# Kernel tuning notes

Measured on AMD Instinct MI355X. Metric: run time of the kernel, lower is better.

## Reference

```python
import jax, jax.numpy as jnp
import numpy as np

L, H, D, N, M, P, C, IMG, B = 12, 12, 768, 197, 3072, 16, 3, 224, 16
SKIP_AT = (3, 6, 9, 12)


def pos_emb(n, d):
    i = jnp.arange(n, dtype=jnp.float32)[:, None]
    j = jnp.arange(d)[None, :]
    je = (j // 2) * 2  # j for even, j-1 for odd
    ang = i / jnp.power(10000.0, je.astype(jnp.float32) / d)
    return jnp.where(j % 2 == 0, jnp.sin(ang), jnp.cos(ang))  # [n, d]


def layer_norm(x, g, b):
    mu = x.mean(-1, keepdims=True)
    var = x.var(-1, keepdims=True)
    return (x - mu) / jnp.sqrt(var + 1e-5) * g + b


def setup_inputs() -> dict:
    key = jax.random.key(0)
    ks = jax.random.split(key, 16)
    s = 0.02
    f32 = jnp.float32
    return {
        "images": jax.random.normal(ks[0], (B, C, IMG, IMG), f32),
        "class_token": jax.random.uniform(ks[1], (1, D), f32),
        "Wp": jax.random.normal(ks[2], (D, P * P * C), f32) * s,
        "bp": jnp.zeros((D,), f32),
        "Wq": jax.random.normal(ks[3], (L, H, D, D), f32) * s,
        "bq": jnp.zeros((L, H, D), f32),
        "Wk": jax.random.normal(ks[4], (L, H, D, D), f32) * s,
        "bk": jnp.zeros((L, H, D), f32),
        "Wv": jax.random.normal(ks[5], (L, H, D, D), f32) * s,
        "bv": jnp.zeros((L, H, D), f32),
        "Wm": jax.random.normal(ks[6], (L, N, H * N), f32) * s,
        "bm": jnp.zeros((L, N), f32),
        "g1": jnp.ones((L, D), f32),
        "be1": jnp.zeros((L, D), f32),
        "W1": jax.random.normal(ks[7], (L, M, D), f32) * s,
        "b1": jnp.zeros((L, M), f32),
        "W2": jax.random.normal(ks[8], (L, D, M), f32) * s,
        "b2": jnp.zeros((L, D), f32),
        "g2": jnp.ones((L, D), f32),
        "be2": jnp.zeros((L, D), f32),
    }


def reference(images, class_token, Wp, bp, Wq, bq, Wk, bk, Wv, bv, Wm, bm,
              g1, be1, W1, b1, W2, b2, g2, be2):
    b = images.shape[0]
    Hn, Wn = IMG // P, IMG // P
    # einops 'b c (patch_x h) (patch_y w) -> b (h w) (patch_x patch_y c)'
    x = images.reshape(b, C, P, Hn, P, Wn).transpose(0, 3, 5, 2, 4, 1)
    patches = x.reshape(b, Hn * Wn, P * P * C)
    tokens = patches @ Wp.T + bp  # [b, N-1, D]
    cls = jnp.broadcast_to(class_token[None], (b, 1, D))
    out = jnp.concatenate([cls, tokens], axis=1) + pos_emb(N, D)[None]
    scale = 1.0 / jnp.sqrt(jnp.float32(N - 1))
    skips = []
    for l in range(L):
        x0 = out
        q = jnp.einsum('bnd,hed->bhne', x0, Wq[l]) + bq[l][None, :, None, :]
        k = jnp.einsum('bnd,hed->bhne', x0, Wk[l]) + bk[l][None, :, None, :]
        v = jnp.einsum('bnd,hed->bhne', x0, Wv[l]) + bv[l][None, :, None, :]
        attn = jax.nn.softmax(jnp.einsum('bhne,bhme->bhnm', q, k) * scale, axis=-1)
        o = jnp.einsum('bhnm,bhme->bhne', attn, v).reshape(b, H * N, D)
        # transpose -> [b, D, H*N], Linear(H*N -> N), transpose back
        msa = jnp.einsum('bfd,nf->bnd', o, Wm[l]) + bm[l][None, :, None]
        x1 = layer_norm(x0 + msa, g1[l], be1[l])
        hdn = jax.nn.gelu(x1 @ W1[l].T + b1[l], approximate=False)
        out = layer_norm(x1 + (hdn @ W2[l].T + b2[l]), g2[l], be2[l])
        if l + 1 in SKIP_AT:
            skips.append(out[:, 1:, :])
    return (out[:, 1:, :], *skips)
```

## Files before the change

kernel.cpp:

```cpp
#include <hip/hip_runtime.h>
#include <cstdint>
#include <cstddef>

typedef __bf16 bf16;
typedef __bf16 bf16x8 __attribute__((ext_vector_type(8)));
typedef float f32x4 __attribute__((ext_vector_type(4)));

#define DEVINL __device__ __forceinline__

typedef const __attribute__((address_space(1))) void* as1cv;
typedef __attribute__((address_space(3))) void* as3v;

DEVINL void gload16(const bf16* g, bf16* l) {
    __builtin_amdgcn_global_load_lds((as1cv)g, (as3v)l, 16, 0, 0);
}

static constexpr int Lh = 12, Hh = 12, Dh = 768, Nh = 197, Mh = 3072, Bh = 16;
static constexpr int BN   = Bh * Nh;
static constexpr int NPAT = Bh * 196;
static constexpr int HD   = Hh * Dh;
static constexpr int QKN  = 2 * HD;
static constexpr int QKV3 = 3 * HD;
static constexpr int NP   = 256;
static constexpr int FHN  = Hh * Nh;
static constexpr int FP   = 2368;
static constexpr size_t SEC = (size_t)Bh * 196 * Dh;
static constexpr long LS3 = (long)QKV3 * Dh;
static constexpr long PART = (long)BN * Dh;

template<int AF32, int BF32, int OUTBF, int BIAS, int ACT, int ZFILL>
__global__ __launch_bounds__(256, 4) void gemm_bt(
    const void* __restrict__ Av, long sAy, long sAz, int lda,
    const void* __restrict__ Bv, long sBy, long sBz, int ldb,
    void* __restrict__ Cv, long sCy, long sCz, int ldc,
    const float* __restrict__ bias, long sBiasY,
    int Mv, int Nv, int K, int tilesN, int kChunk)
{
    __shared__ __align__(16) bf16 Asm[128 * 64];
    __shared__ __align__(16) bf16 Bsm[128 * 64];
    const int tm = blockIdx.x / tilesN, tn = blockIdx.x % tilesN;
    const long aoff = (long)blockIdx.y * sAy + (long)blockIdx.z * sAz + (long)tm * 128 * lda;
    const long boff = (long)blockIdx.y * sBy + (long)blockIdx.z * sBz + (long)tn * 128 * ldb;
    const int tid = threadIdx.x;
    const int lane = tid & 63, wid = tid >> 6;
    const int ar = tid >> 3, ac = (tid & 7) << 3;
    const bf16* Ag = (const bf16*)Av + aoff + (long)ar * lda + ac;
    const bf16* Bg = (const bf16*)Bv + boff + (long)ar * ldb + ac;
    const float* Af = (const float*)Av + aoff + (long)ar * lda + ac;
    const float* Bf = (const float*)Bv + boff + (long)ar * ldb + ac;
    bf16* lA = Asm + wid * 512;
    bf16* lB = Bsm + wid * 512;
    const int mw = (wid >> 1) * 64, nw = (wid & 1) * 64;
    const int fr = lane & 15, fq = lane >> 4;
    const int kBeg = kChunk ? blockIdx.y * kChunk : 0;
    const int kEnd = kChunk ? min(K, kBeg + kChunk) : K;
    f32x4 acc[4][4] = {};
    for (int k0 = kBeg; k0 < kEnd; k0 += 64) {
        if (AF32) {
#pragma unroll
            for (int jp = 0; jp < 4; jp++) {
                const float* p0 = Af + (long)jp * 32 * lda + k0;
                f32x4 a0 = *(const f32x4*)p0, a1 = *(const f32x4*)(p0 + 4);
                bf16x8 r0;
#pragma unroll
                for (int i = 0; i < 4; i++) { r0[i] = (bf16)a0[i]; r0[i + 4] = (bf16)a1[i]; }
                *(bf16x8*)&Asm[(jp * 32 + ar) * 64 + ac] = r0;
            }
        } else {
#pragma unroll
            for (int jp = 0; jp < 4; jp++)
                gload16(Ag + (long)jp * 32 * lda + k0, lA + jp * 2048);
        }
        if (BF32) {
#pragma unroll
            for (int jp = 0; jp < 4; jp++) {
                const float* p0 = Bf + (long)jp * 32 * ldb + k0;
                f32x4 a0 = *(const f32x4*)p0, a1 = *(const f32x4*)(p0 + 4);
                bf16x8 r0;
#pragma unroll
                for (int i = 0; i < 4; i++) { r0[i] = (bf16)a0[i]; r0[i + 4] = (bf16)a1[i]; }
                *(bf16x8*)&Bsm[(jp * 32 + ar) * 64 + ac] = r0;
            }
        } else {
#pragma unroll
            for (int jp = 0; jp < 4; jp++)
                gload16(Bg + (long)jp * 32 * ldb + k0, lB + jp * 2048);
        }
        __syncthreads();
#pragma unroll
        for (int ks = 0; ks < 2; ks++) {
            bf16x8 af[4], bv[4];
#pragma unroll
            for (int i = 0; i < 4; i++)
                af[i] = *(const bf16x8*)&Asm[(mw + i * 16 + fr) * 64 + (ks << 5) + (fq << 3)];
#pragma unroll
            for (int j = 0; j < 4; j++)
                bv[j] = *(const bf16x8*)&Bsm[(nw + j * 16 + fr) * 64 + (ks << 5) + (fq << 3)];
#pragma unroll
            for (int i = 0; i < 4; i++)
#pragma unroll
                for (int j = 0; j < 4; j++)
                    acc[i][j] = __builtin_amdgcn_mfma_f32_16x16x32_bf16(af[i], bv[j], acc[i][j], 0, 0, 0);
        }
        __syncthreads();
    }
    const long cb = (long)blockIdx.y * sCy + (long)blockIdx.z * sCz;
    const float* biasp = bias ? bias + (long)blockIdx.y * sBiasY : nullptr;
#pragma unroll
    for (int i = 0; i < 4; i++) {
        const int row0 = tm * 128 + mw + i * 16 + fq * 4;
#pragma unroll
        for (int j = 0; j < 4; j++) {
            const int col = tn * 128 + nw + j * 16 + fr;
            const bool cok = (col < Nv);
            if (!cok && !ZFILL) continue;
            float bc = (BIAS == 1 && cok) ? biasp[col] : 0.f;
#pragma unroll
            for (int r = 0; r < 4; r++) {
                const int rr = row0 + r;
                if (rr >= Mv) continue;
                float v;
                if (cok) {
                    v = acc[i][j][r];
                    if (BIAS == 1) v += bc;
                    if (BIAS == 2) v += biasp[rr];
                    if (ACT) v = 0.5f * v * (1.f + erff(v * 0.70710678118654752f));
                } else v = 0.f;
                const long ci = cb + (long)rr * ldc + col;
                if (OUTBF) ((bf16*)Cv)[ci] = (bf16)v;
                else       ((float*)Cv)[ci] = v;
            }
        }
    }
}

__global__ __launch_bounds__(512, 2) void qksoft_k(
    const bf16* __restrict__ qkb, bf16* __restrict__ P)
{
    __shared__ __align__(16) bf16 Qs[128 * 32];
    __shared__ __align__(16) bf16 Ks[256 * 32];
    __shared__ float redM[2][64][4];
    __shared__ float redS[2][64][4];
    const int rt = blockIdx.x, h = blockIdx.y, b = blockIdx.z;
    const int tid = threadIdx.x;
    const int lane = tid & 63, wid = tid >> 6;
    const int wr = wid >> 2, wc = wid & 3;
    const int fr = lane & 15, fq = lane >> 4;
    const int ar = tid >> 2, ac = (tid & 3) << 3;
    const bf16* Qg = qkb + ((size_t)b * Nh + rt * 128 + ar) * QKV3 + h * Dh + ac;
    const bf16* Kg = qkb + ((size_t)b * Nh + ar) * QKV3 + HD + h * Dh + ac;
    bf16* lQ = Qs + wid * 512;
    bf16* lK = Ks + wid * 512;
    f32x4 acc[4][4] = {};
    for (int k0 = 0; k0 < 768; k0 += 32) {
        gload16(Qg + k0, lQ);
        gload16(Kg + k0, lK);
        gload16(Kg + (size_t)128 * QKV3 + k0, lK + 4096);
        __syncthreads();
        bf16x8 af[4], bv[4];
#pragma unroll
        for (int i = 0; i < 4; i++) af[i] = *(const bf16x8*)&Qs[(wr * 64 + i * 16 + fr) * 32 + (fq << 3)];
#pragma unroll
        for (int j = 0; j < 4; j++) bv[j] = *(const bf16x8*)&Ks[(wc * 64 + j * 16 + fr) * 32 + (fq << 3)];
#pragma unroll
        for (int i = 0; i < 4; i++)
#pragma unroll
            for (int j = 0; j < 4; j++)
                acc[i][j] = __builtin_amdgcn_mfma_f32_16x16x32_bf16(af[i], bv[j], acc[i][j], 0, 0, 0);
        __syncthreads();
    }
    const float scale = 1.f / 14.f;
    float mx[4][4];
#pragma unroll
    for (int i = 0; i < 4; i++)
#pragma unroll
        for (int r = 0; r < 4; r++) {
            float m0 = -3e30f;
#pragma unroll
            for (int j = 0; j < 4; j++) {
                const int m = wc * 64 + j * 16 + fr;
                float v = (m < Nh) ? acc[i][j][r] * scale : -3e30f;
                acc[i][j][r] = v;
                m0 = fmaxf(m0, v);
            }
            m0 = fmaxf(m0, __shfl_xor(m0, 1));
            m0 = fmaxf(m0, __shfl_xor(m0, 2));
            m0 = fmaxf(m0, __shfl_xor(m0, 4));
            m0 = fmaxf(m0, __shfl_xor(m0, 8));
            mx[i][r] = m0;
        }
    if (fr == 0) {
#pragma unroll
        for (int i = 0; i < 4; i++)
#pragma unroll
            for (int r = 0; r < 4; r++) redM[wr][i * 16 + fq * 4 + r][wc] = mx[i][r];
    }
    __syncthreads();
    float sm[4][4];
#pragma unroll
    for (int i = 0; i < 4; i++)
#pragma unroll
        for (int r = 0; r < 4; r++) {
            const int row = i * 16 + fq * 4 + r;
            const float rm = fmaxf(fmaxf(redM[wr][row][0], redM[wr][row][1]),
                                   fmaxf(redM[wr][row][2], redM[wr][row][3]));
            float s0 = 0.f;
#pragma unroll
            for (int j = 0; j < 4; j++) {
                const float e = expf(acc[i][j][r] - rm);
                acc[i][j][r] = e;
                s0 += e;
            }
            s0 += __shfl_xor(s0, 1);
            s0 += __shfl_xor(s0, 2);
            s0 += __shfl_xor(s0, 4);
            s0 += __shfl_xor(s0, 8);
            sm[i][r] = s0;
        }
    if (fr == 0) {
#pragma unroll
        for (int i = 0; i < 4; i++)
#pragma unroll
            for (int r = 0; r < 4; r++) redS[wr][i * 16 + fq * 4 + r][wc] = sm[i][r];
    }
    __syncthreads();
    bf16* Pb = P + ((size_t)(b * Hh + h) * NP + rt * 128) * NP;
#pragma unroll
    for (int i = 0; i < 4; i++)
#pragma unroll
        for (int r = 0; r < 4; r++) {
            const int row = i * 16 + fq * 4 + r;
            const float s = redS[wr][row][0] + redS[wr][row][1] + redS[wr][row][2] + redS[wr][row][3];
            const float inv = 1.f / s;
#pragma unroll
            for (int j = 0; j < 4; j++)
                Pb[(size_t)(wr * 64 + row) * NP + wc * 64 + j * 16 + fr] = (bf16)(acc[i][j][r] * inv);
        }
}

__global__ __launch_bounds__(256) void vtrans_k(const bf16* __restrict__ qkv, bf16* __restrict__ vT) {
    __shared__ bf16 t[64][72];
    const int eb = (blockIdx.x >> 2) << 6;
    const int nb = (blockIdx.x & 3) << 6;
    const int h = blockIdx.y, b = blockIdx.z;
    const int tid = threadIdx.x;
    const int lr = tid >> 2;
    const int lc = (tid & 3) << 4;
    const int n = nb + lr;
    if (n < Nh) {
        const bf16* src = qkv + (size_t)(b * Nh + n) * QKV3 + 2 * HD + h * Dh + eb + lc;
        *(bf16x8*)&t[lr][lc] = *(const bf16x8*)src;
        *(bf16x8*)&t[lr][lc + 8] = *(const bf16x8*)(src + 8);
    } else {
        bf16x8 z = {};
        *(bf16x8*)&t[lr][lc] = z; *(bf16x8*)&t[lr][lc + 8] = z;
    }
    __syncthreads();
    bf16* dst = vT + ((size_t)(b * Hh + h) * Dh + eb + lr) * NP + nb + lc;
    bf16x8 o0, o1;
#pragma unroll
    for (int j = 0; j < 8; j++) { o0[j] = t[lc + j][lr]; o1[j] = t[lc + 8 + j][lr]; }
    *(bf16x8*)dst = o0; *(bf16x8*)(dst + 8) = o1;
}

__global__ __launch_bounds__(256) void cvt_k(const float* __restrict__ in, bf16* __restrict__ out, long n) {
    const long i = ((long)blockIdx.x * 256 + threadIdx.x) * 8;
    if (i >= n) return;
    f32x4 a = *(const f32x4*)(in + i);
    f32x4 b = *(const f32x4*)(in + i + 4);
    bf16x8 r;
#pragma unroll
    for (int j = 0; j < 4; j++) { r[j] = (bf16)a[j]; r[j + 4] = (bf16)b[j]; }
    *(bf16x8*)(out + i) = r;
}

__global__ __launch_bounds__(256) void cvt_s_k(const float* __restrict__ in, bf16* __restrict__ out,
                                               long perLayer, long dstStride, long dstOff, long total) {
    const long i = ((long)blockIdx.x * 256 + threadIdx.x) * 8;
    if (i >= total) return;
    const long l = i / perLayer, r = i % perLayer;
    f32x4 a = *(const f32x4*)(in + i);
    f32x4 b = *(const f32x4*)(in + i + 4);
    bf16x8 v;
#pragma unroll
    for (int j = 0; j < 4; j++) { v[j] = (bf16)a[j]; v[j + 4] = (bf16)b[j]; }
    *(bf16x8*)(out + l * dstStride + dstOff + r) = v;
}

__global__ void qkvbias_k(const float* __restrict__ bq, const float* __restrict__ bk,
                          const float* __restrict__ bv, float* __restrict__ dst) {
    const int idx = blockIdx.x * 256 + threadIdx.x;
    if (idx >= Lh * QKV3) return;
    const int l = idx / QKV3, c = idx % QKV3;
    float v;
    if (c < HD) v = bq[l * HD + c];
    else if (c < 2 * HD) v = bk[l * HD + c - HD];
    else v = bv[l * HD + c - 2 * HD];
    dst[idx] = v;
}

__global__ void patch_k(const float* __restrict__ images, bf16* __restrict__ patches) {
    const long idx = (long)blockIdx.x * 256 + threadIdx.x;
    if (idx >= (long)NPAT * Dh) return;
    const int r = (int)(idx / Dh), f = (int)(idx % Dh);
    const int b = r / 196, pi = r % 196, h = pi / 14, w = pi % 14;
    const int px = f / 48, rem = f % 48, py = rem / 3, c = rem % 3;
    patches[idx] = (bf16)images[(((long)(b * 3 + c) * 224) + px * 14 + h) * 224 + py * 14 + w];
}

__global__ void assemble_k(const float* __restrict__ tokens, const float* __restrict__ cls,
                           float* __restrict__ x, bf16* __restrict__ xbf) {
    const long idx = (long)blockIdx.x * 256 + threadIdx.x;
    if (idx >= (long)BN * Dh) return;
    const int r = (int)(idx / Dh), d = (int)(idx % Dh);
    const int b = r / Nh, n = r % Nh;
    const int je = d & ~1;
    const float ang = (float)n / powf(10000.f, (float)je / 768.f);
    const float pe = (d & 1) ? cosf(ang) : sinf(ang);
    const float val = (n == 0) ? (cls[d] + pe)
                               : (tokens[((long)b * 196 + (n - 1)) * Dh + d] + pe);
    x[idx] = val;
    xbf[idx] = (bf16)val;
}

__global__ void wmpad_k(const float* __restrict__ Wm, bf16* __restrict__ WmP) {
    const long idx = (long)blockIdx.x * 256 + threadIdx.x;
    if (idx >= (long)Lh * 256 * FP) return;
    const int l = (int)(idx / (256 * FP));
    const int rem = (int)(idx % (256 * FP));
    const int n = rem / FP, f = rem % FP;
    bf16 v = (bf16)0.f;
    if (n < Nh && f < FHN) v = (bf16)Wm[((long)l * Nh + n) * FHN + f];
    WmP[idx] = v;
}

__global__ void otpad_k(bf16* __restrict__ oT, int cb) {
    const int idx = blockIdx.x * 256 + threadIdx.x;
    if (idx >= cb * Dh * 4) return;
    const int b = idx / (Dh * 4), rem = idx % (Dh * 4), e = rem / 4, f = rem % 4;
    oT[((long)b * Dh + e) * FP + FHN + f] = (bf16)0.f;
}

__global__ __launch_bounds__(256) void softmax_k(const float* __restrict__ S, bf16* __restrict__ P) {
    const int tid = threadIdx.x, lane = tid & 63, wv = tid >> 6;
    const long rr = (long)blockIdx.x * 4 + wv;
    const int bh = (int)(rr / Nh), n = (int)(rr % Nh);
    const float* s = S + ((long)bh * Nh + n) * NP;
    bf16* p = P + ((long)bh * NP + n) * NP;
    float v[4]; float mx = -1e30f;
#pragma unroll
    for (int i = 0; i < 4; i++) {
        const int c = lane + i * 64;
        const float t = (c < Nh) ? s[c] * (1.f / 14.f) : -1e30f;
        v[i] = t; mx = fmaxf(mx, t);
    }
    for (int o = 32; o; o >>= 1) mx = fmaxf(mx, __shfl_xor(mx, o));
    float sum = 0.f;
#pragma unroll
    for (int i = 0; i < 4; i++) {
        const int c = lane + i * 64;
        v[i] = (c < Nh) ? expf(v[i] - mx) : 0.f;
        sum += v[i];
    }
    for (int o = 32; o; o >>= 1) sum += __shfl_xor(sum, o);
    const float inv = 1.f / sum;
#pragma unroll
    for (int i = 0; i < 4; i++) p[lane + i * 64] = (bf16)(v[i] * inv);
}

template<int BIAS_ROW, int NPART>
__global__ __launch_bounds__(256) void add_ln_k(
    const float* __restrict__ in1, const float* __restrict__ in2, long pstride,
    const float* __restrict__ bias, const float* __restrict__ gamma, const float* __restrict__ beta,
    float* __restrict__ outF, bf16* __restrict__ outBF,
    float* __restrict__ dst0, float* __restrict__ dst1)
{
    const int r = blockIdx.x;
    const int b = r / Nh, n = r % Nh;
    const long base = (long)r * Dh;
    const int tid = threadIdx.x;
    const float rowb = BIAS_ROW ? bias[n] : 0.f;
    float v[3]; float s = 0.f, s2 = 0.f;
#pragma unroll
    for (int i = 0; i < 3; i++) {
        const int d = tid + 256 * i;
        float t = in1[base + d] + (BIAS_ROW ? rowb : bias[d]);
#pragma unroll
        for (int pp = 0; pp < NPART; pp++) t += in2[pp * pstride + base + d];
        v[i] = t; s += t; s2 += t * t;
    }
    for (int o = 32; o; o >>= 1) { s += __shfl_xor(s, o); s2 += __shfl_xor(s2, o); }
    __shared__ float red[8];
    const int lane = tid & 63, wv = tid >> 6;
    if (lane == 0) { red[wv] = s; red[4 + wv] = s2; }
    __syncthreads();
    s  = red[0] + red[1] + red[2] + red[3];
    s2 = red[4] + red[5] + red[6] + red[7];
    const float mu = s * (1.f / 768.f);
    const float var = s2 * (1.f / 768.f) - mu * mu;
    const float rs = rsqrtf(var + 1e-5f);
    const long ob = ((long)b * 196 + (n - 1)) * Dh;
#pragma unroll
    for (int i = 0; i < 3; i++) {
        const int d = tid + 256 * i;
        const float y = (v[i] - mu) * rs * gamma[d] + beta[d];
        outF[base + d] = y;
        outBF[base + d] = (bf16)y;
        if (n > 0) {
            if (dst0) dst0[ob + d] = y;
            if (dst1) dst1[ob + d] = y;
        }
    }
}

static inline size_t al256(size_t x) { return (x + 255) & ~(size_t)255; }

extern "C" void kernel_launch(void* const* d_in, const int* in_sizes, int n_in,
                              void* d_out, int out_size, void* d_ws, size_t ws_size,
                              hipStream_t stream) {
    (void)in_sizes; (void)n_in; (void)out_size;
    const float* images = (const float*)d_in[0];
    const float* cls    = (const float*)d_in[1];
    const float* Wp     = (const float*)d_in[2];
    const float* bp     = (const float*)d_in[3];
    const float* Wq     = (const float*)d_in[4];
    const float* bq     = (const float*)d_in[5];
    const float* Wk     = (const float*)d_in[6];
    const float* bk     = (const float*)d_in[7];
    const float* Wv     = (const float*)d_in[8];
    const float* bv     = (const float*)d_in[9];
    const float* Wm     = (const float*)d_in[10];
    const float* bm     = (const float*)d_in[11];
    const float* g1     = (const float*)d_in[12];
    const float* be1    = (const float*)d_in[13];
    const float* W1     = (const float*)d_in[14];
    const float* b1     = (const float*)d_in[15];
    const float* W2     = (const float*)d_in[16];
    const float* b2     = (const float*)d_in[17];
    const float* g2     = (const float*)d_in[18];
    const float* be2    = (const float*)d_in[19];
    float* out = (float*)d_out;

    const size_t xB    = al256(3152ull * 768 * 4);
    const size_t xbfB  = al256(3328ull * 768 * 2);
    const size_t x1B   = al256(3152ull * 768 * 4);
    const size_t x1bfB = al256(3200ull * 768 * 2);
    const size_t msaB  = al256(4ull * PART * 4);
    const size_t mlp2B = al256(4ull * PART * 4);
    const size_t wmpB  = al256(12ull * 256 * FP * 2);
    const size_t biasB = al256((size_t)Lh * QKV3 * 4);
    const size_t persistB = xB + xbfB + x1B + x1bfB + msaB + mlp2B + wmpB + biasB;
    const size_t hdnB  = al256(3200ull * 3072 * 2);
    const size_t preB  = al256(3200ull * 768 * 2) + al256(3136ull * 768 * 4);
    const size_t wqkvB = al256((size_t)Lh * HD * Dh * 2);
    const size_t w12B  = al256((size_t)Lh * Mh * Dh * 2);
    const size_t wpB   = al256(768ull * 768 * 2);
    const size_t weightsB = 3 * wqkvB + 2 * w12B + wpB;

    const size_t qkvbB = al256(3328ull * QKV3 * 2);
    const size_t vtBf  = al256((size_t)Bh * Hh * Dh * NP * 2);
    const size_t pBf   = al256((size_t)Bh * Hh * NP * NP * 2);
    const size_t otBf  = al256((size_t)Bh * Dh * FP * 2);
    size_t chunkF = qkvbB + vtBf + pBf + otBf;
    if (chunkF < hdnB) chunkF = hdnB;
    if (chunkF < preB) chunkF = preB;
    const size_t margin = (size_t)(8u << 20);
    const bool fused = (chunkF + persistB + weightsB + margin <= ws_size);

    auto chunk_bytes = [&](int cb, size_t& qbB_o, size_t& vtB_o, size_t& sB_o) -> size_t {
        const size_t qbRows = (size_t)((cb * 197 + 127) / 128 + 1) * 128;
        size_t qbB = al256(qbRows * HD * 2);
        size_t vtB = al256((size_t)cb * Hh * Dh * NP * 2);
        size_t sB  = al256((size_t)cb * Hh * Nh * NP * 4);
        size_t c = 2 * qbB + vtB + sB;
        if (c < hdnB) c = hdnB;
        if (c < preB) c = preB;
        qbB_o = qbB; vtB_o = vtB; sB_o = sB;
        return c;
    };
    int CB = 16; bool useCvt = true;
    size_t qbB, vtB, sB, chunkB;
    if (fused) {
        chunkB = chunkF; qbB = vtB = sB = 0;
    } else {
        for (;;) {
            chunkB = chunk_bytes(CB, qbB, vtB, sB);
            if (chunkB + persistB + weightsB + margin <= ws_size) break;
            if (CB == 1) { useCvt = false; break; }
            CB >>= 1;
        }
        if (!useCvt) {
            CB = 16;
            for (;;) {
                chunkB = chunk_bytes(CB, qbB, vtB, sB);
                if (chunkB + persistB + margin <= ws_size || CB == 1) break;
                CB >>= 1;
            }
        }
    }

    char* wsb = (char*)d_ws;
    bf16*  qkvb = (bf16*)wsb;
    bf16*  vT2  = (bf16*)(wsb + qkvbB);
    bf16*  P2   = (bf16*)(wsb + qkvbB + vtBf);
    bf16*  oT2  = (bf16*)(wsb + qkvbB + vtBf + pBf);
    bf16*  qb  = (bf16*)wsb;
    bf16*  kb  = (bf16*)(wsb + qbB);
    bf16*  vTf = (bf16*)(wsb + 2 * qbB);
    float* S   = (float*)(wsb + 2 * qbB + vtB);
    bf16*  vT  = fused ? vT2 : vTf;
    bf16*  oT  = fused ? oT2 : qb;
    bf16*  P   = fused ? P2  : kb;
    bf16*  hdn = (bf16*)wsb;
    bf16*  patches = (bf16*)wsb;
    float* tokens  = (float*)(wsb + al256(3200ull * 768 * 2));
    char* p = wsb + chunkB;
    float* x    = (float*)p; p += xB;
    bf16*  xbf  = (bf16*) p; p += xbfB;
    float* x1   = (float*)p; p += x1B;
    bf16*  x1bf = (bf16*) p; p += x1bfB;
    float* msaP = (float*)p; p += msaB;
    float* mlp2P= (float*)p; p += mlp2B;
    bf16*  WmP  = (bf16*) p; p += wmpB;
    float* qkvbias = (float*)p; p += biasB;
    bf16 *WqkvB = nullptr, *W1B = nullptr, *W2B = nullptr, *WpB = nullptr;
    const bool cvt = fused || useCvt;
    if (cvt) {
        WqkvB = (bf16*)p; p += 3 * wqkvB;
        W1B  = (bf16*)p; p += w12B;
        W2B  = (bf16*)p; p += w12B;
        WpB  = (bf16*)p; p += wpB;
    }

    if (cvt) {
        const long nqkv = (long)Lh * HD * Dh;
        const long n12  = (long)Lh * Mh * Dh;
        const int gq = (int)((nqkv / 8 + 255) / 256);
        const int g12 = (int)((n12 / 8 + 255) / 256);
        cvt_s_k<<<gq, 256, 0, stream>>>(Wq, WqkvB, (long)HD * Dh, LS3, 0, nqkv);
        cvt_s_k<<<gq, 256, 0, stream>>>(Wk, WqkvB, (long)HD * Dh, LS3, (long)HD * Dh, nqkv);
        cvt_s_k<<<gq, 256, 0, stream>>>(Wv, WqkvB, (long)HD * Dh, LS3, 2L * HD * Dh, nqkv);
        cvt_k<<<g12, 256, 0, stream>>>(W1, W1B, n12);
        cvt_k<<<g12, 256, 0, stream>>>(W2, W2B, n12);
        cvt_k<<<(768 * 768 / 8 + 255) / 256, 256, 0, stream>>>(Wp, WpB, 768 * 768);
        qkvbias_k<<<(Lh * QKV3 + 255) / 256, 256, 0, stream>>>(bq, bk, bv, qkvbias);
    }

    patch_k<<<9408, 256, 0, stream>>>(images, patches);
    if (cvt)
        gemm_bt<0, 0, 0, 1, 0, 0><<<dim3(25 * 6), 256, 0, stream>>>(
            patches, 0, 0, 768, WpB, 0, 0, 768, tokens, 0, 0, 768, bp, 0, NPAT, 768, 768, 6, 0);
    else
        gemm_bt<0, 1, 0, 1, 0, 0><<<dim3(25 * 6), 256, 0, stream>>>(
            patches, 0, 0, 768, Wp, 0, 0, 768, tokens, 0, 0, 768, bp, 0, NPAT, 768, 768, 6, 0);
    assemble_k<<<9456, 256, 0, stream>>>(tokens, cls, x, xbf);
    wmpad_k<<<28416, 256, 0, stream>>>(Wm, WmP);
    if (fused) otpad_k<<<16 * 12, 256, 0, stream>>>(oT2, 16);

    const int NCH = 16 / CB;
    const int tilesQ = (CB * 197 + 127) / 128;

    for (int l = 0; l < 12; l++) {
        const float* Wq_l = Wq + (size_t)l * HD * Dh;
        const float* Wk_l = Wk + (size_t)l * HD * Dh;
        const float* Wv_l = Wv + (size_t)l * HD * Dh;
        const bf16* Wqkv_l = cvt ? WqkvB + (size_t)l * LS3 : nullptr;
        const bf16* WqB_l = Wqkv_l;
        const bf16* WkB_l = cvt ? Wqkv_l + (size_t)HD * Dh : nullptr;
        const bf16* WvB_l = cvt ? Wqkv_l + 2 * (size_t)HD * Dh : nullptr;
        const float* bq_l = bq + (size_t)l * HD;
        const float* bk_l = bk + (size_t)l * HD;
        const float* bv_l = bv + (size_t)l * HD;
        const bf16*  WmP_l = WmP + (size_t)l * 256 * FP;
        const float* bm_l = bm + (size_t)l * Nh;
        const float* g1_l = g1 + (size_t)l * Dh;  const float* be1_l = be1 + (size_t)l * Dh;
        const float* W1_l = W1 + (size_t)l * Mh * Dh; const float* b1_l = b1 + (size_t)l * Mh;
        const float* W2_l = W2 + (size_t)l * Dh * Mh; const float* b2_l = b2 + (size_t)l * Dh;
        const bf16* W1B_l = cvt ? W1B + (size_t)l * Mh * Dh : nullptr;
        const bf16* W2B_l = cvt ? W2B + (size_t)l * Mh * Dh : nullptr;
        const float* g2_l = g2 + (size_t)l * Dh;  const float* be2_l = be2 + (size_t)l * Dh;

        if (fused) {
            gemm_bt<0, 0, 1, 1, 0, 0><<<dim3(25 * 216), 256, 0, stream>>>(
                xbf, 0, 0, 768, Wqkv_l, 0, 0, 768, qkvb, 0, 0, QKV3,
                qkvbias + (size_t)l * QKV3, 0, BN, QKV3, 768, 216, 0);
            vtrans_k<<<dim3(48, 12, 16), 256, 0, stream>>>(qkvb, vT);
            qksoft_k<<<dim3(2, Hh, Bh), 512, 0, stream>>>(qkvb, P);
            gemm_bt<0, 0, 1, 0, 0, 0><<<dim3(12, 12, 16), 256, 0, stream>>>(
                vT, (long)Dh * NP, (long)Hh * Dh * NP, NP,
                P, (long)NP * NP, (long)Hh * NP * NP, NP,
                oT, (long)Nh, (long)Dh * FP, FP,
                nullptr, 0, Dh, Nh, NP, 2, 0);
            gemm_bt<0, 0, 0, 0, 0, 0><<<dim3(12, 4, 16), 256, 0, stream>>>(
                WmP_l, 0, 0, FP,
                oT, 0, (long)Dh * FP, FP,
                msaP, PART, (long)Nh * Dh, Dh,
                nullptr, 0, Nh, Dh, FP, 6, 640);
        } else {
            for (int c = 0; c < NCH; c++) {
                const size_t r0 = (size_t)c * CB * Nh;
                if (useCvt) {
                    gemm_bt<0, 0, 1, 1, 0, 0><<<dim3(tilesQ * 72), 256, 0, stream>>>(
                        xbf + r0 * Dh, 0, 0, 768, WqB_l, 0, 0, 768, qb, 0, 0, HD, bq_l, 0, CB * Nh, HD, 768, 72, 0);
                    gemm_bt<0, 0, 1, 1, 0, 0><<<dim3(tilesQ * 72), 256, 0, stream>>>(
                        xbf + r0 * Dh, 0, 0, 768, WkB_l, 0, 0, 768, kb, 0, 0, HD, bk_l, 0, CB * Nh, HD, 768, 72, 0);
                    gemm_bt<0, 0, 1, 2, 0, 1><<<dim3(12, 12, CB), 256, 0, stream>>>(
                        WvB_l, (long)Dh * Dh, 0, 768,
                        xbf + r0 * Dh, 0, (long)Nh * Dh, 768,
                        vT, (long)Dh * NP, (long)Hh * Dh * NP, NP,
                        bv_l, Dh, 768, Nh, 768, 2, 0);
                } else {
                    gemm_bt<0, 1, 1, 1, 0, 0><<<dim3(tilesQ * 72), 256, 0, stream>>>(
                        xbf + r0 * Dh, 0, 0, 768, Wq_l, 0, 0, 768, qb, 0, 0, HD, bq_l, 0, CB * Nh, HD, 768, 72, 0);
                    gemm_bt<0, 1, 1, 1, 0, 0><<<dim3(tilesQ * 72), 256, 0, stream>>>(
                        xbf + r0 * Dh, 0, 0, 768, Wk_l, 0, 0, 768, kb, 0, 0, HD, bk_l, 0, CB * Nh, HD, 768, 72, 0);
                    gemm_bt<1, 0, 1, 2, 0, 1><<<dim3(12, 12, CB), 256, 0, stream>>>(
                        Wv_l, (long)Dh * Dh, 0, 768,
                        xbf + r0 * Dh, 0, (long)Nh * Dh, 768,
                        vT, (long)Dh * NP, (long)Hh * Dh * NP, NP,
                        bv_l, Dh, 768, Nh, 768, 2, 0);
                }
                gemm_bt<0, 0, 0, 0, 0, 0><<<dim3(4, 12, CB), 256, 0, stream>>>(
                    qb, Dh, (long)Nh * HD, HD,
                    kb, Dh, (long)Nh * HD, HD,
                    S, (long)Nh * NP, (long)Hh * Nh * NP, NP,
                    nullptr, 0, Nh, Nh, 768, 2, 0);
                softmax_k<<<CB * 591, 256, 0, stream>>>(S, P);
                otpad_k<<<CB * 12, 256, 0, stream>>>(oT, CB);
                gemm_bt<0, 0, 1, 0, 0, 0><<<dim3(12, 12, CB), 256, 0, stream>>>(
                    vT, (long)Dh * NP, (long)Hh * Dh * NP, NP,
                    P, (long)NP * NP, (long)Hh * NP * NP, NP,
                    oT, (long)Nh, (long)Dh * FP, FP,
                    nullptr, 0, Dh, Nh, NP, 2, 0);
                gemm_bt<0, 0, 0, 0, 0, 0><<<dim3(12, 4, CB), 256, 0, stream>>>(
                    WmP_l, 0, 0, FP,
                    oT, 0, (long)Dh * FP, FP,
                    msaP + r0 * Dh, PART, (long)Nh * Dh, Dh,
                    nullptr, 0, Nh, Dh, FP, 6, 640);
            }
        }
        add_ln_k<1, 4><<<BN, 256, 0, stream>>>(x, msaP, PART, bm_l, g1_l, be1_l, x1, x1bf, nullptr, nullptr);
        if (cvt) {
            gemm_bt<0, 0, 1, 1, 1, 0><<<dim3(25 * 24), 256, 0, stream>>>(
                x1bf, 0, 0, 768, W1B_l, 0, 0, 768, hdn, 0, 0, Mh, b1_l, 0, BN, Mh, 768, 24, 0);
            gemm_bt<0, 0, 0, 0, 0, 0><<<dim3(25 * 6, 4, 1), 256, 0, stream>>>(
                hdn, 0, 0, Mh, W2B_l, 0, 0, Mh, mlp2P, PART, 0, Dh, nullptr, 0, BN, Dh, Mh, 6, 768);
        } else {
            gemm_bt<0, 1, 1, 1, 1, 0><<<dim3(25 * 24), 256, 0, stream>>>(
                x1bf, 0, 0, 768, W1_l, 0, 0, 768, hdn, 0, 0, Mh, b1_l, 0, BN, Mh, 768, 24, 0);
            gemm_bt<0, 1, 0, 0, 0, 0><<<dim3(25 * 6, 4, 1), 256, 0, stream>>>(
                hdn, 0, 0, Mh, W2_l, 0, 0, Mh, mlp2P, PART, 0, Dh, nullptr, 0, BN, Dh, Mh, 6, 768);
        }
        float* d0 = nullptr; float* d1 = nullptr;
        if (l == 2)  d0 = out + 1 * SEC;
        if (l == 5)  d0 = out + 2 * SEC;
        if (l == 8)  d0 = out + 3 * SEC;
        if (l == 11) { d0 = out; d1 = out + 4 * SEC; }
        add_ln_k<0, 4><<<BN, 256, 0, stream>>>(x1, mlp2P, PART, b2_l, g2_l, be2_l, x, xbf, d0, d1);
    }
}
```

Baseline: 5.879 ms.

## XOR-swizzle LDS tiles in GEMM and widen QK kernel K-step to 64

```diff
diff --git a/kernel.cpp b/kernel.cpp
--- a/kernel.cpp
+++ b/kernel.cpp
@@ -43,9 +43,11 @@
     const long boff = (long)blockIdx.y * sBy + (long)blockIdx.z * sBz + (long)tn * 128 * ldb;
     const int tid = threadIdx.x;
     const int lane = tid & 63, wid = tid >> 6;
-    const int ar = tid >> 3, ac = (tid & 7) << 3;
-    const bf16* Ag = (const bf16*)Av + aoff + (long)ar * lda + ac;
-    const bf16* Bg = (const bf16*)Bv + boff + (long)ar * ldb + ac;
+    const int ar = tid >> 3;
+    const int ac = (tid & 7) << 3;
+    const int acs = (((tid & 7) ^ ((tid >> 3) & 7)) << 3);
+    const bf16* Ag = (const bf16*)Av + aoff + (long)ar * lda + acs;
+    const bf16* Bg = (const bf16*)Bv + boff + (long)ar * ldb + acs;
     const float* Af = (const float*)Av + aoff + (long)ar * lda + ac;
     const float* Bf = (const float*)Bv + boff + (long)ar * ldb + ac;
     bf16* lA = Asm + wid * 512;
@@ -64,7 +66,7 @@
                 bf16x8 r0;
 #pragma unroll
                 for (int i = 0; i < 4; i++) { r0[i] = (bf16)a0[i]; r0[i + 4] = (bf16)a1[i]; }
-                *(bf16x8*)&Asm[(jp * 32 + ar) * 64 + ac] = r0;
+                *(bf16x8*)&Asm[(jp * 32 + ar) * 64 + (ac ^ ((ar & 7) << 3))] = r0;
             }
         } else {
 #pragma unroll
@@ -79,7 +81,7 @@
                 bf16x8 r0;
 #pragma unroll
                 for (int i = 0; i < 4; i++) { r0[i] = (bf16)a0[i]; r0[i + 4] = (bf16)a1[i]; }
-                *(bf16x8*)&Bsm[(jp * 32 + ar) * 64 + ac] = r0;
+                *(bf16x8*)&Bsm[(jp * 32 + ar) * 64 + (ac ^ ((ar & 7) << 3))] = r0;
             }
         } else {
 #pragma unroll
@@ -91,11 +93,15 @@
         for (int ks = 0; ks < 2; ks++) {
             bf16x8 af[4], bv[4];
 #pragma unroll
-            for (int i = 0; i < 4; i++)
-                af[i] = *(const bf16x8*)&Asm[(mw + i * 16 + fr) * 64 + (ks << 5) + (fq << 3)];
-#pragma unroll
-            for (int j = 0; j < 4; j++)
-                bv[j] = *(const bf16x8*)&Bsm[(nw + j * 16 + fr) * 64 + (ks << 5) + (fq << 3)];
+            for (int i = 0; i < 4; i++) {
+                const int rl = mw + i * 16 + fr;
+                af[i] = *(const bf16x8*)&Asm[rl * 64 + ((((ks << 2) | fq) ^ (rl & 7)) << 3)];
+            }
+#pragma unroll
+            for (int j = 0; j < 4; j++) {
+                const int rl = nw + j * 16 + fr;
+                bv[j] = *(const bf16x8*)&Bsm[rl * 64 + ((((ks << 2) | fq) ^ (rl & 7)) << 3)];
+            }
 #pragma unroll
             for (int i = 0; i < 4; i++)
 #pragma unroll
@@ -137,8 +143,8 @@
 __global__ __launch_bounds__(512, 2) void qksoft_k(
     const bf16* __restrict__ qkb, bf16* __restrict__ P)
 {
-    __shared__ __align__(16) bf16 Qs[128 * 32];
-    __shared__ __align__(16) bf16 Ks[256 * 32];
+    __shared__ __align__(16) bf16 Qs[128 * 64];
+    __shared__ __align__(16) bf16 Ks[256 * 64];
     __shared__ float redM[2][64][4];
     __shared__ float redS[2][64][4];
     const int rt = blockIdx.x, h = blockIdx.y, b = blockIdx.z;
@@ -146,27 +152,40 @@
     const int lane = tid & 63, wid = tid >> 6;
     const int wr = wid >> 2, wc = wid & 3;
     const int fr = lane & 15, fq = lane >> 4;
-    const int ar = tid >> 2, ac = (tid & 3) << 3;
-    const bf16* Qg = qkb + ((size_t)b * Nh + rt * 128 + ar) * QKV3 + h * Dh + ac;
-    const bf16* Kg = qkb + ((size_t)b * Nh + ar) * QKV3 + HD + h * Dh + ac;
+    const int ar = tid >> 3;
+    const int acs = (((tid & 7) ^ ((tid >> 3) & 7)) << 3);
+    const bf16* Qg = qkb + ((size_t)b * Nh + rt * 128 + ar) * QKV3 + h * Dh + acs;
+    const bf16* Kg = qkb + ((size_t)b * Nh + ar) * QKV3 + HD + h * Dh + acs;
     bf16* lQ = Qs + wid * 512;
     bf16* lK = Ks + wid * 512;
     f32x4 acc[4][4] = {};
-    for (int k0 = 0; k0 < 768; k0 += 32) {
-        gload16(Qg + k0, lQ);
-        gload16(Kg + k0, lK);
-        gload16(Kg + (size_t)128 * QKV3 + k0, lK + 4096);
+    for (int k0 = 0; k0 < 768; k0 += 64) {
+#pragma unroll
+        for (int jp = 0; jp < 2; jp++)
+            gload16(Qg + (size_t)jp * 64 * QKV3 + k0, lQ + jp * 4096);
+#pragma unroll
+        for (int jp = 0; jp < 4; jp++)
+            gload16(Kg + (size_t)jp * 64 * QKV3 + k0, lK + jp * 4096);
         __syncthreads();
-        bf16x8 af[4], bv[4];
-#pragma unroll
-        for (int i = 0; i < 4; i++) af[i] = *(const bf16x8*)&Qs[(wr * 64 + i * 16 + fr) * 32 + (fq << 3)];
-#pragma unroll
-        for (int j = 0; j < 4; j++) bv[j] = *(const bf16x8*)&Ks[(wc * 64 + j * 16 + fr) * 32 + (fq << 3)];
-#pragma unroll
-        for (int i = 0; i < 4; i++)
-#pragma unroll
-            for (int j = 0; j < 4; j++)
-                acc[i][j] = __builtin_amdgcn_mfma_f32_16x16x32_bf16(af[i], bv[j], acc[i][j], 0, 0, 0);
+#pragma unroll
+        for (int ks = 0; ks < 2; ks++) {
+            bf16x8 af[4], bv[4];
+#pragma unroll
+            for (int i = 0; i < 4; i++) {
+                const int rl = wr * 64 + i * 16 + fr;
+                af[i] = *(const bf16x8*)&Qs[rl * 64 + ((((ks << 2) | fq) ^ (rl & 7)) << 3)];
+            }
+#pragma unroll
+            for (int j = 0; j < 4; j++) {
+                const int rl = wc * 64 + j * 16 + fr;
+                bv[j] = *(const bf16x8*)&Ks[rl * 64 + ((((ks << 2) | fq) ^ (rl & 7)) << 3)];
+            }
+#pragma unroll
+            for (int i = 0; i < 4; i++)
+#pragma unroll
+                for (int j = 0; j < 4; j++)
+                    acc[i][j] = __builtin_amdgcn_mfma_f32_16x16x32_bf16(af[i], bv[j], acc[i][j], 0, 0, 0);
+        }
         __syncthreads();
     }
     const float scale = 1.f / 14.f;
```

New measurement: 5.580 ms (median of 2 runs). -5.1%, faster.
